# Kernel tuning notes

Measured on AMD Instinct MI355X. Metric: run time of the kernel, lower is better.

Reference implementation:

```python
import jax, jax.numpy as jnp
import numpy as np

N_NODES = 100000
N_EDGES = 1000000
D_NODE = 64
D_EDGE = 64
D_IN = 2 * D_NODE + D_EDGE  # 192, concat of src n_f, s_f, dst n_f
D_OUT = 64


def setup_inputs() -> dict:
    key = jax.random.key(0)
    k1, k2, k3, k4, k5 = jax.random.split(key, 5)
    node_feat = jax.random.normal(k1, (N_NODES, D_NODE), dtype=jnp.float32)
    edge_feat = jax.random.normal(k2, (N_EDGES, D_EDGE), dtype=jnp.float32)
    src_idx = jax.random.randint(k3, (N_EDGES,), 0, N_NODES, dtype=jnp.int64) if jax.config.jax_enable_x64 else jax.random.randint(k3, (N_EDGES,), 0, N_NODES, dtype=jnp.int32)
    dst_idx = jax.random.randint(k4, (N_EDGES,), 0, N_NODES, dtype=jnp.int32)
    src_idx = src_idx.astype(jnp.int32)
    # Kaiming-ish init for the edge MLP (torch Linear default scale ~ 1/sqrt(fan_in))
    W = jax.random.normal(k5, (D_IN, D_OUT), dtype=jnp.float32) / np.sqrt(D_IN)
    b = jnp.zeros((D_OUT,), dtype=jnp.float32)
    return {"node_feat": node_feat, "edge_feat": edge_feat,
            "src_idx": src_idx, "dst_idx": dst_idx, "W": W, "b": b}


def reference(node_feat, edge_feat, src_idx, dst_idx, W, b):
    # EdgeApplyModule.forward: cat([src n_f, s_f, dst n_f], dim=1) -> mlp -> e_f
    feat = jnp.concatenate(
        [node_feat[src_idx], edge_feat, node_feat[dst_idx]], axis=1)  # [E, 192]
    e_f = jax.nn.relu(feat @ W + b)  # Linear(192->64, bias) + ReLU, dropout=0 (eval)
    return e_f
```

## Files before the change

### kernel.cpp

```cpp
#include <hip/hip_runtime.h>
#include <hip/hip_bf16.h>


typedef __attribute__((ext_vector_type(8))) short short8;
typedef __attribute__((ext_vector_type(4))) float f32x4;

#define D 64
#define DIN 192
#define BM 64
#define GRID 2048

__device__ __forceinline__ short bf_bits(float f) {
  __hip_bfloat16 h = __float2bfloat16(f);
  union { __hip_bfloat16 b; short s; } u; u.b = h;
  return u.s;
}

__global__ void prep_W_kernel(const float* __restrict__ W,
                              unsigned short* __restrict__ wsB) {
  int i = blockIdx.x * blockDim.x + threadIdx.x;
  if (i >= DIN * D) return;
  int k = i >> 6;
  int n = i & 63;
  int t = k >> 5;
  int g = (k >> 3) & 3;
  int s = k & 7;
  int c = n >> 4;
  int l = g * 16 + (n & 15);
  wsB[(((t << 2) + c) * 64 + l) * 8 + s] = (unsigned short)bf_bits(W[i]);
}

__global__ __launch_bounds__(256) void edge_mlp_kernel(
    const float* __restrict__ node_feat,
    const float* __restrict__ edge_feat,
    const int*   __restrict__ src_idx,
    const int*   __restrict__ dst_idx,
    const unsigned short* __restrict__ wsB,
    const float* __restrict__ bias,
    float* __restrict__ out,
    int nE) {
  const int tid = threadIdx.x;
  const int w = tid >> 6;
  const int l = tid & 63;
  const int g = l >> 4;
  const int r = l & 15;

  const short8* B = reinterpret_cast<const short8*>(wsB);

  float bn0 = bias[0 * 16 + r];
  float bn1 = bias[1 * 16 + r];
  float bn2 = bias[2 * 16 + r];
  float bn3 = bias[3 * 16 + r];

  const int nChunks = (nE + BM - 1) / BM;

  for (int chunk = blockIdx.x; chunk < nChunks; chunk += gridDim.x) {
    const long base = (long)chunk * BM + w * 16;
    int e = (int)base + r;
    int eL = e < nE ? e : nE - 1;

    const int si = src_idx[eL];
    const int di = dst_idx[eL];
    const float* pSrc = node_feat + (size_t)si * D;
    const float* pEdg = edge_feat + (size_t)eL * D;
    const float* pDst = node_feat + (size_t)di * D;

    f32x4 acc0 = {0.f, 0.f, 0.f, 0.f};
    f32x4 acc1 = {0.f, 0.f, 0.f, 0.f};
    f32x4 acc2 = {0.f, 0.f, 0.f, 0.f};
    f32x4 acc3 = {0.f, 0.f, 0.f, 0.f};

    #pragma unroll
    for (int t = 0; t < 6; ++t) {
      const float* seg = (t < 2) ? pSrc : (t < 4) ? pEdg : pDst;
      const float* p = seg + (t & 1) * 32 + g * 8;
      float4 x = *reinterpret_cast<const float4*>(p);
      float4 y = *reinterpret_cast<const float4*>(p + 4);
      short8 a;
      a[0] = bf_bits(x.x); a[1] = bf_bits(x.y);
      a[2] = bf_bits(x.z); a[3] = bf_bits(x.w);
      a[4] = bf_bits(y.x); a[5] = bf_bits(y.y);
      a[6] = bf_bits(y.z); a[7] = bf_bits(y.w);

      short8 b0 = B[(t * 4 + 0) * 64 + l];
      short8 b1 = B[(t * 4 + 1) * 64 + l];
      short8 b2 = B[(t * 4 + 2) * 64 + l];
      short8 b3 = B[(t * 4 + 3) * 64 + l];
      acc0 = __builtin_amdgcn_mfma_f32_16x16x32_bf16(a, b0, acc0, 0, 0, 0);
      acc1 = __builtin_amdgcn_mfma_f32_16x16x32_bf16(a, b1, acc1, 0, 0, 0);
      acc2 = __builtin_amdgcn_mfma_f32_16x16x32_bf16(a, b2, acc2, 0, 0, 0);
      acc3 = __builtin_amdgcn_mfma_f32_16x16x32_bf16(a, b3, acc3, 0, 0, 0);
    }

    f32x4 accs[4] = {acc0, acc1, acc2, acc3};
    float bns[4] = {bn0, bn1, bn2, bn3};
    #pragma unroll
    for (int c = 0; c < 4; ++c) {
      const int n = c * 16 + r;
      #pragma unroll
      for (int j = 0; j < 4; ++j) {
        const long eo = base + g * 4 + j;
        if (eo < nE) {
          float v = accs[c][j] + bns[c];
          out[eo * D + n] = v > 0.f ? v : 0.f;
        }
      }
    }
  }
}

extern "C" void kernel_launch(void* const* d_in, const int* in_sizes, int n_in,
                              void* d_out, int out_size, void* d_ws, size_t ws_size,
                              hipStream_t stream) {
  const float* node_feat = (const float*)d_in[0];
  const float* edge_feat = (const float*)d_in[1];
  const int*   src_idx   = (const int*)d_in[2];
  const int*   dst_idx   = (const int*)d_in[3];
  const float* W         = (const float*)d_in[4];
  const float* bias      = (const float*)d_in[5];
  float* out = (float*)d_out;
  unsigned short* wsB = (unsigned short*)d_ws;

  const int nE = in_sizes[2];

  hipLaunchKernelGGL(prep_W_kernel, dim3((DIN * D + 255) / 256), dim3(256), 0,
                     stream, W, wsB);

  const int nChunks = (nE + BM - 1) / BM;
  const int grid = nChunks < GRID ? nChunks : GRID;
  hipLaunchKernelGGL(edge_mlp_kernel, dim3(grid), dim3(256), 0, stream,
                     node_feat, edge_feat, src_idx, dst_idx, wsB, bias, out, nE);
}
```

Measured before the change: 499.6 us.

## Software-pipeline gathers with register prefetch of next chunk's rows and indices

Restructures the grid-stride loop so the node/edge feature gathers for the next chunk are issued into registers before the MFMA work of the current chunk, and the indices for the chunk after that are loaded one step further ahead. This is meant to hide the latency of the random gathers behind compute and stores. It also raises launch bounds to request 4 blocks per CU and uses an opaque zero offset to keep the weight loads from being hoisted out of the loop. The extra register buffers may raise register pressure or cause spills.

```diff
diff --git a/kernel.cpp b/kernel.cpp
--- a/kernel.cpp
+++ b/kernel.cpp
@@ -30,7 +30,7 @@
   wsB[(((t << 2) + c) * 64 + l) * 8 + s] = (unsigned short)bf_bits(W[i]);
 }
 
-__global__ __launch_bounds__(256) void edge_mlp_kernel(
+__global__ __launch_bounds__(256, 4) void edge_mlp_kernel(
     const float* __restrict__ node_feat,
     const float* __restrict__ edge_feat,
     const int*   __restrict__ src_idx,
@@ -44,64 +44,118 @@
   const int l = tid & 63;
   const int g = l >> 4;
   const int r = l & 15;
+  const int rowIC = w * 16 + r;
+  const int gofs = g * 8;
 
   const short8* B = reinterpret_cast<const short8*>(wsB);
+  const int nChunks = (nE + BM - 1) / BM;
+  const int G = gridDim.x;
 
-  float bn0 = bias[0 * 16 + r];
-  float bn1 = bias[1 * 16 + r];
-  float bn2 = bias[2 * 16 + r];
-  float bn3 = bias[3 * 16 + r];
+  const float bn0 = bias[r], bn1 = bias[16 + r], bn2 = bias[32 + r],
+              bn3 = bias[48 + r];
 
-  const int nChunks = (nE + BM - 1) / BM;
+  float4 X[12];
+  int si1, di1, ec1;
 
-  for (int chunk = blockIdx.x; chunk < nChunks; chunk += gridDim.x) {
-    const long base = (long)chunk * BM + w * 16;
-    int e = (int)base + r;
-    int eL = e < nE ? e : nE - 1;
+  int c = blockIdx.x;
 
-    const int si = src_idx[eL];
-    const int di = dst_idx[eL];
-    const float* pSrc = node_feat + (size_t)si * D;
-    const float* pEdg = edge_feat + (size_t)eL * D;
-    const float* pDst = node_feat + (size_t)di * D;
+  {
+    long e0 = (long)c * BM + rowIC;
+    int eL = e0 < nE ? (int)e0 : nE - 1;
+    si1 = src_idx[eL];
+    di1 = dst_idx[eL];
+    ec1 = eL;
+  }
+  {
+    const float* pS = node_feat + (size_t)si1 * D + gofs;
+    const float* pE = edge_feat + (size_t)ec1 * D + gofs;
+    const float* pD = node_feat + (size_t)di1 * D + gofs;
+    X[0]  = *reinterpret_cast<const float4*>(pS);
+    X[1]  = *reinterpret_cast<const float4*>(pS + 4);
+    X[2]  = *reinterpret_cast<const float4*>(pS + 32);
+    X[3]  = *reinterpret_cast<const float4*>(pS + 36);
+    X[4]  = *reinterpret_cast<const float4*>(pE);
+    X[5]  = *reinterpret_cast<const float4*>(pE + 4);
+    X[6]  = *reinterpret_cast<const float4*>(pE + 32);
+    X[7]  = *reinterpret_cast<const float4*>(pE + 36);
+    X[8]  = *reinterpret_cast<const float4*>(pD);
+    X[9]  = *reinterpret_cast<const float4*>(pD + 4);
+    X[10] = *reinterpret_cast<const float4*>(pD + 32);
+    X[11] = *reinterpret_cast<const float4*>(pD + 36);
+  }
+  {
+    long e1 = (long)(c + G) * BM + rowIC;
+    int eL = e1 < nE ? (int)e1 : nE - 1;
+    si1 = src_idx[eL];
+    di1 = dst_idx[eL];
+    ec1 = eL;
+  }
 
-    f32x4 acc0 = {0.f, 0.f, 0.f, 0.f};
-    f32x4 acc1 = {0.f, 0.f, 0.f, 0.f};
-    f32x4 acc2 = {0.f, 0.f, 0.f, 0.f};
-    f32x4 acc3 = {0.f, 0.f, 0.f, 0.f};
+  for (; c < nChunks; c += G) {
+    short8 A[6];
+    #pragma unroll
+    for (int t = 0; t < 6; ++t) {
+      float4 x = X[2 * t], y = X[2 * t + 1];
+      A[t][0] = bf_bits(x.x); A[t][1] = bf_bits(x.y);
+      A[t][2] = bf_bits(x.z); A[t][3] = bf_bits(x.w);
+      A[t][4] = bf_bits(y.x); A[t][5] = bf_bits(y.y);
+      A[t][6] = bf_bits(y.z); A[t][7] = bf_bits(y.w);
+    }
+
+    if (c + G < nChunks) {
+      const float* pS = node_feat + (size_t)si1 * D + gofs;
+      const float* pE = edge_feat + (size_t)ec1 * D + gofs;
+      const float* pD = node_feat + (size_t)di1 * D + gofs;
+      X[0]  = *reinterpret_cast<const float4*>(pS);
+      X[1]  = *reinterpret_cast<const float4*>(pS + 4);
+      X[2]  = *reinterpret_cast<const float4*>(pS + 32);
+      X[3]  = *reinterpret_cast<const float4*>(pS + 36);
+      X[4]  = *reinterpret_cast<const float4*>(pE);
+      X[5]  = *reinterpret_cast<const float4*>(pE + 4);
+      X[6]  = *reinterpret_cast<const float4*>(pE + 32);
+      X[7]  = *reinterpret_cast<const float4*>(pE + 36);
+      X[8]  = *reinterpret_cast<const float4*>(pD);
+      X[9]  = *reinterpret_cast<const float4*>(pD + 4);
+      X[10] = *reinterpret_cast<const float4*>(pD + 32);
+      X[11] = *reinterpret_cast<const float4*>(pD + 36);
+
+      long e2 = (long)(c + 2 * G) * BM + rowIC;
+      int eL = e2 < nE ? (int)e2 : nE - 1;
+      si1 = src_idx[eL];
+      di1 = dst_idx[eL];
+      ec1 = eL;
+    }
+
+    int bofs = 0;
+    asm volatile("" : "+v"(bofs));
+    const short8* B2 = B + bofs;
+
+    f32x4 acc[4];
+    #pragma unroll
+    for (int cc = 0; cc < 4; ++cc) acc[cc] = (f32x4){0.f, 0.f, 0.f, 0.f};
 
     #pragma unroll
     for (int t = 0; t < 6; ++t) {
-      const float* seg = (t < 2) ? pSrc : (t < 4) ? pEdg : pDst;
-      const float* p = seg + (t & 1) * 32 + g * 8;
-      float4 x = *reinterpret_cast<const float4*>(p);
-      float4 y = *reinterpret_cast<const float4*>(p + 4);
-      short8 a;
-      a[0] = bf_bits(x.x); a[1] = bf_bits(x.y);
-      a[2] = bf_bits(x.z); a[3] = bf_bits(x.w);
-      a[4] = bf_bits(y.x); a[5] = bf_bits(y.y);
-      a[6] = bf_bits(y.z); a[7] = bf_bits(y.w);
-
-      short8 b0 = B[(t * 4 + 0) * 64 + l];
-      short8 b1 = B[(t * 4 + 1) * 64 + l];
-      short8 b2 = B[(t * 4 + 2) * 64 + l];
-      short8 b3 = B[(t * 4 + 3) * 64 + l];
-      acc0 = __builtin_amdgcn_mfma_f32_16x16x32_bf16(a, b0, acc0, 0, 0, 0);
-      acc1 = __builtin_amdgcn_mfma_f32_16x16x32_bf16(a, b1, acc1, 0, 0, 0);
-      acc2 = __builtin_amdgcn_mfma_f32_16x16x32_bf16(a, b2, acc2, 0, 0, 0);
-      acc3 = __builtin_amdgcn_mfma_f32_16x16x32_bf16(a, b3, acc3, 0, 0, 0);
+      short8 b0 = B2[(t * 4 + 0) * 64 + l];
+      short8 b1 = B2[(t * 4 + 1) * 64 + l];
+      short8 b2 = B2[(t * 4 + 2) * 64 + l];
+      short8 b3 = B2[(t * 4 + 3) * 64 + l];
+      acc[0] = __builtin_amdgcn_mfma_f32_16x16x32_bf16(A[t], b0, acc[0], 0, 0, 0);
+      acc[1] = __builtin_amdgcn_mfma_f32_16x16x32_bf16(A[t], b1, acc[1], 0, 0, 0);
+      acc[2] = __builtin_amdgcn_mfma_f32_16x16x32_bf16(A[t], b2, acc[2], 0, 0, 0);
+      acc[3] = __builtin_amdgcn_mfma_f32_16x16x32_bf16(A[t], b3, acc[3], 0, 0, 0);
     }
 
-    f32x4 accs[4] = {acc0, acc1, acc2, acc3};
-    float bns[4] = {bn0, bn1, bn2, bn3};
+    const long baseW = (long)c * BM + w * 16;
+    const float bns[4] = {bn0, bn1, bn2, bn3};
     #pragma unroll
-    for (int c = 0; c < 4; ++c) {
-      const int n = c * 16 + r;
+    for (int cc = 0; cc < 4; ++cc) {
+      const int n = cc * 16 + r;
       #pragma unroll
       for (int j = 0; j < 4; ++j) {
-        const long eo = base + g * 4 + j;
+        long eo = baseW + g * 4 + j;
         if (eo < nE) {
-          float v = accs[c][j] + bns[c];
+          float v = acc[cc][j] + bns[cc];
           out[eo * D + n] = v > 0.f ? v : 0.f;
         }
       }
```

After: 541.9 us. +8.5%, slower.
